# Optimization experiments

Measured on AMD Instinct MI355X. Metric: run time of the kernel, lower is better.

## Reference

```python
import jax, jax.numpy as jnp
import numpy as np

N = 8192
F_IN = 256
F_OUT = 128
SLOPE = 0.2
NEG_INF = -9000000000000000.0


def setup_inputs() -> dict:
    key = jax.random.key(0)
    k1, k2, k3, k4, k5 = jax.random.split(key, 5)
    x = jax.random.normal(k1, (N, F_IN), dtype=jnp.float32)
    adj = jax.random.randint(k2, (N, N), 0, 2).astype(jnp.float32)
    W = jax.random.normal(k3, (F_IN, F_OUT), dtype=jnp.float32) * (1.0 / np.sqrt(F_IN))
    a_src = jax.random.normal(k4, (F_OUT,), dtype=jnp.float32) * (1.0 / np.sqrt(F_OUT))
    a_dst = jax.random.normal(k5, (F_OUT,), dtype=jnp.float32) * (1.0 / np.sqrt(F_OUT))
    return {"x": x, "adj": adj, "W": W, "a_src": a_src, "a_dst": a_dst}


def reference(x, adj, W, a_src, a_dst):
    # h: (N, F_OUT)
    h = x @ W
    f_src = h @ a_src  # (N,)
    f_dst = h @ a_dst  # (N,)
    # additive attention scores: (N, N)
    e = f_src[:, None] + f_dst[None, :]
    e = jnp.where(e >= 0, e, SLOPE * e)  # leaky_relu
    e = jnp.where(adj > 0, e, NEG_INF)
    alpha = jax.nn.softmax(e, axis=1)  # (N, N)
    return alpha @ h  # (N, F_OUT)
```

## Files before the change

### kernel.cpp

```cpp
#include <hip/hip_runtime.h>
#include <hip/hip_bf16.h>

#define NN 8192
#define FIN 256
#define FO 128
#define JCHUNK 2048
#define NSTEP 32
#define L2E 1.4426950408889634f
#define C2  0.28853900817779268f

typedef __bf16 bf16x8 __attribute__((ext_vector_type(8)));
typedef __bf16 bf16x2 __attribute__((ext_vector_type(2)));
typedef float  f32x4  __attribute__((ext_vector_type(4)));

__global__ __launch_bounds__(256) void k_proj(
    const float* __restrict__ x, const float* __restrict__ W,
    const float* __restrict__ a_src, const float* __restrict__ a_dst,
    __bf16* __restrict__ Bp, float* __restrict__ f_src,
    float* __restrict__ g1, float* __restrict__ g2)
{
  __shared__ float xs[16 * FIN];
  __shared__ float fs[16], fd[16];
  const int tid = threadIdx.x;
  const int i0 = blockIdx.x * 16;

  const float4* xg = (const float4*)(x + (size_t)i0 * FIN);
  float4* xs4 = (float4*)xs;
  #pragma unroll
  for (int t = 0; t < 4; t++) xs4[tid + 256 * t] = xg[tid + 256 * t];
  if (tid < 16) { fs[tid] = 0.f; fd[tid] = 0.f; }
  __syncthreads();

  const int cq = tid & 31;
  const int rg = tid >> 5;
  const int c0 = cq * 4;
  const int r0 = rg * 2;
  float acc0[4] = {0.f,0.f,0.f,0.f};
  float acc1[4] = {0.f,0.f,0.f,0.f};
  const float* xr0 = xs + r0 * FIN;
  const float* xr1 = xs + (r0 + 1) * FIN;

  for (int k = 0; k < FIN; k += 4) {
    float4 xa = *(const float4*)(xr0 + k);
    float4 xb = *(const float4*)(xr1 + k);
    #pragma unroll
    for (int kk = 0; kk < 4; kk++) {
      float4 wv = *(const float4*)(W + (size_t)(k + kk) * FO + c0);
      float xav = ((const float*)&xa)[kk];
      float xbv = ((const float*)&xb)[kk];
      acc0[0] += xav * wv.x; acc0[1] += xav * wv.y;
      acc0[2] += xav * wv.z; acc0[3] += xav * wv.w;
      acc1[0] += xbv * wv.x; acc1[1] += xbv * wv.y;
      acc1[2] += xbv * wv.z; acc1[3] += xbv * wv.w;
    }
  }

  float4 as = *(const float4*)(a_src + c0);
  float4 ad = *(const float4*)(a_dst + c0);
  float ps0 = acc0[0]*as.x + acc0[1]*as.y + acc0[2]*as.z + acc0[3]*as.w;
  float ps1 = acc1[0]*as.x + acc1[1]*as.y + acc1[2]*as.z + acc1[3]*as.w;
  float pd0 = acc0[0]*ad.x + acc0[1]*ad.y + acc0[2]*ad.z + acc0[3]*ad.w;
  float pd1 = acc1[0]*ad.x + acc1[1]*ad.y + acc1[2]*ad.z + acc1[3]*ad.w;
  atomicAdd(&fs[r0],     ps0);
  atomicAdd(&fs[r0 + 1], ps1);
  atomicAdd(&fd[r0],     pd0);
  atomicAdd(&fd[r0 + 1], pd1);

  const int j0 = i0 + r0;
  const int kg = j0 >> 5;
  const int q  = (j0 >> 3) & 3;
  const int t0 = j0 & 7;
  #pragma unroll
  for (int c = 0; c < 4; c++) {
    const int n = c0 + c;
    bf16x2 v;
    v[0] = (__bf16)acc0[c];
    v[1] = (__bf16)acc1[c];
    size_t idx = ((size_t)(kg * 8 + (n >> 4)) * 64 + q * 16 + (n & 15)) * 8 + t0;
    *(bf16x2*)(Bp + idx) = v;
  }
  __syncthreads();
  if (tid < 16) {
    float d = fd[tid];
    f_src[i0 + tid] = fs[tid];
    g1[i0 + tid] = __builtin_amdgcn_exp2f(d * L2E);
    g2[i0 + tid] = __builtin_amdgcn_exp2f(d * C2);
  }
}

__global__ __launch_bounds__(256, 2) void k_attn(
    const float* __restrict__ adj, const __bf16* __restrict__ Bp,
    const float* __restrict__ f_src, const float* __restrict__ g1,
    const float* __restrict__ g2, float* __restrict__ out)
{
  __shared__ float accbuf[16 * FO];
  __shared__ float lred[16];
  const int tid = threadIdx.x;
  const int i0 = blockIdx.x * 16;

  ((float4*)accbuf)[tid]       = (float4){0.f, 0.f, 0.f, 0.f};
  ((float4*)accbuf)[tid + 256] = (float4){0.f, 0.f, 0.f, 0.f};
  if (tid < 16) lred[tid] = 0.f;

  const int w = tid >> 6;
  const int lane = tid & 63;
  const int m = lane & 15;
  const int q = lane >> 4;
  const int jbase = w * JCHUNK;

  const float s  = f_src[i0 + m];
  const float F1 = __builtin_amdgcn_exp2f(s * L2E);
  const float F2 = __builtin_amdgcn_exp2f(s * C2);

  f32x4 acc[8];
  #pragma unroll
  for (int t = 0; t < 8; t++) acc[t] = (f32x4){0.f, 0.f, 0.f, 0.f};
  float psum = 0.f;

  const float* adjp = adj + (size_t)(i0 + m) * NN + jbase + q * 8;
  const float* g1p = g1 + jbase + q * 8;
  const float* g2p = g2 + jbase + q * 8;
  const __bf16* bb = Bp + (size_t)(jbase >> 5) * 4096 + lane * 8;

  __syncthreads();

  float4 cur0 = *(const float4*)(adjp + 0);
  float4 cur1 = *(const float4*)(adjp + 4);
  float4 cur2 = *(const float4*)(adjp + 32);
  float4 cur3 = *(const float4*)(adjp + 36);

  #pragma unroll 2
  for (int st = 0; st < NSTEP; ++st) {
    float4 nxt0, nxt1, nxt2, nxt3;
    if (st < NSTEP - 1) {
      const float* ap = adjp + (st + 1) * 64;
      nxt0 = *(const float4*)(ap + 0);
      nxt1 = *(const float4*)(ap + 4);
      nxt2 = *(const float4*)(ap + 32);
      nxt3 = *(const float4*)(ap + 36);
    }
    #pragma unroll
    for (int g = 0; g < 2; ++g) {
      const int ko = st * 64 + g * 32;
      float4 a0 = g ? cur2 : cur0;
      float4 a1 = g ? cur3 : cur1;
      float4 u0 = *(const float4*)(g1p + ko);
      float4 u1 = *(const float4*)(g1p + ko + 4);
      float4 v0 = *(const float4*)(g2p + ko);
      float4 v1 = *(const float4*)(g2p + ko + 4);
      float p0 = (a0.x > 0.f) ? fmaxf(F1 * u0.x, F2 * v0.x) : 0.f;
      float p1 = (a0.y > 0.f) ? fmaxf(F1 * u0.y, F2 * v0.y) : 0.f;
      float p2 = (a0.z > 0.f) ? fmaxf(F1 * u0.z, F2 * v0.z) : 0.f;
      float p3 = (a0.w > 0.f) ? fmaxf(F1 * u0.w, F2 * v0.w) : 0.f;
      float p4 = (a1.x > 0.f) ? fmaxf(F1 * u1.x, F2 * v1.x) : 0.f;
      float p5 = (a1.y > 0.f) ? fmaxf(F1 * u1.y, F2 * v1.y) : 0.f;
      float p6 = (a1.z > 0.f) ? fmaxf(F1 * u1.z, F2 * v1.z) : 0.f;
      float p7 = (a1.w > 0.f) ? fmaxf(F1 * u1.w, F2 * v1.w) : 0.f;
      psum += ((p0 + p1) + (p2 + p3)) + ((p4 + p5) + (p6 + p7));

      bf16x8 af;
      af[0] = (__bf16)p0; af[1] = (__bf16)p1; af[2] = (__bf16)p2; af[3] = (__bf16)p3;
      af[4] = (__bf16)p4; af[5] = (__bf16)p5; af[6] = (__bf16)p6; af[7] = (__bf16)p7;

      const __bf16* bs = bb + (size_t)(st * 2 + g) * 4096;
      #pragma unroll
      for (int nt = 0; nt < 8; nt++) {
        bf16x8 bfrag = *(const bf16x8*)(bs + nt * 512);
        acc[nt] = __builtin_amdgcn_mfma_f32_16x16x32_bf16(af, bfrag, acc[nt], 0, 0, 0);
      }
    }
    if (st < NSTEP - 1) { cur0 = nxt0; cur1 = nxt1; cur2 = nxt2; cur3 = nxt3; }
  }

  psum += __shfl_xor(psum, 16);
  psum += __shfl_xor(psum, 32);
  if (lane < 16) atomicAdd(&lred[lane], psum);

  #pragma unroll
  for (int nt = 0; nt < 8; nt++) {
    #pragma unroll
    for (int r = 0; r < 4; r++) {
      atomicAdd(&accbuf[(q * 4 + r) * FO + nt * 16 + m], acc[nt][r]);
    }
  }
  __syncthreads();

  #pragma unroll
  for (int t = 0; t < 2; t++) {
    const int idx = tid + t * 256;
    const float inv = 1.0f / lred[idx >> 5];
    float4 v = ((const float4*)accbuf)[idx];
    float4 o;
    o.x = v.x * inv; o.y = v.y * inv; o.z = v.z * inv; o.w = v.w * inv;
    ((float4*)(out + (size_t)i0 * FO))[idx] = o;
  }
}

extern "C" void kernel_launch(void* const* d_in, const int* in_sizes, int n_in,
                              void* d_out, int out_size, void* d_ws, size_t ws_size,
                              hipStream_t stream) {
  const float* x     = (const float*)d_in[0];
  const float* adj   = (const float*)d_in[1];
  const float* W     = (const float*)d_in[2];
  const float* a_src = (const float*)d_in[3];
  const float* a_dst = (const float*)d_in[4];
  float* out = (float*)d_out;

  char* ws = (char*)d_ws;
  __bf16* Bp   = (__bf16*)ws;
  float* f_src = (float*)(ws + 2097152);
  float* g1    = (float*)(ws + 2097152 + 32768);
  float* g2    = (float*)(ws + 2097152 + 65536);

  hipLaunchKernelGGL(k_proj, dim3(512), dim3(256), 0, stream,
                     x, W, a_src, a_dst, Bp, f_src, g1, g2);
  hipLaunchKernelGGL(k_attn, dim3(512), dim3(256), 0, stream,
                     adj, Bp, f_src, g1, g2, out);
}
```

Before: 469.7 us.

## Tile attention over 64 rows with split-K across blocks and global atomic reduction

Each attention block now covers 64 rows and a quarter of the columns, so every B-fragment load from the projected features feeds four MFMAs instead of one. The g1/g2 vectors are staged in shared memory, and adj is read with nontemporal loads. Partial numerators and row sums from the four column splits are merged with global atomics into a zeroed buffer, and a new divide kernel applies the normalisation. This cuts repeated reads of the bf16 feature matrix, but adds a memset, a third kernel, float-atomic traffic, heavy register pressure from 32 accumulators, and less latency hiding for adj since the software prefetch is gone.

```diff
diff --git a/kernel.cpp b/kernel.cpp
--- a/kernel.cpp
+++ b/kernel.cpp
@@ -4,8 +4,6 @@
 #define NN 8192
 #define FIN 256
 #define FO 128
-#define JCHUNK 2048
-#define NSTEP 32
 #define L2E 1.4426950408889634f
 #define C2  0.28853900817779268f
 
@@ -91,109 +89,139 @@
 __global__ __launch_bounds__(256, 2) void k_attn(
     const float* __restrict__ adj, const __bf16* __restrict__ Bp,
     const float* __restrict__ f_src, const float* __restrict__ g1,
-    const float* __restrict__ g2, float* __restrict__ out)
+    const float* __restrict__ g2, float* __restrict__ num,
+    float* __restrict__ lsum)
 {
-  __shared__ float accbuf[16 * FO];
-  __shared__ float lred[16];
+  __shared__ float G1s[2048], G2s[2048];
+  __shared__ float accbuf[64 * FO];
+  __shared__ float lred[64];
   const int tid = threadIdx.x;
-  const int i0 = blockIdx.x * 16;
-
-  ((float4*)accbuf)[tid]       = (float4){0.f, 0.f, 0.f, 0.f};
-  ((float4*)accbuf)[tid + 256] = (float4){0.f, 0.f, 0.f, 0.f};
-  if (tid < 16) lred[tid] = 0.f;
+  const int rb = blockIdx.x >> 2;
+  const int ks = blockIdx.x & 3;
+  const int i0 = rb * 64;
+  const int cb = ks * 2048;
+
+  {
+    const float4* s1 = (const float4*)(g1 + cb);
+    const float4* s2 = (const float4*)(g2 + cb);
+    ((float4*)G1s)[tid]       = s1[tid];
+    ((float4*)G1s)[tid + 256] = s1[tid + 256];
+    ((float4*)G2s)[tid]       = s2[tid];
+    ((float4*)G2s)[tid + 256] = s2[tid + 256];
+  }
+  #pragma unroll
+  for (int t = 0; t < 8; t++)
+    ((float4*)accbuf)[tid + 256 * t] = (float4){0.f, 0.f, 0.f, 0.f};
+  if (tid < 64) lred[tid] = 0.f;
 
   const int w = tid >> 6;
   const int lane = tid & 63;
   const int m = lane & 15;
   const int q = lane >> 4;
-  const int jbase = w * JCHUNK;
-
-  const float s  = f_src[i0 + m];
-  const float F1 = __builtin_amdgcn_exp2f(s * L2E);
-  const float F2 = __builtin_amdgcn_exp2f(s * C2);
-
-  f32x4 acc[8];
-  #pragma unroll
-  for (int t = 0; t < 8; t++) acc[t] = (f32x4){0.f, 0.f, 0.f, 0.f};
-  float psum = 0.f;
-
-  const float* adjp = adj + (size_t)(i0 + m) * NN + jbase + q * 8;
-  const float* g1p = g1 + jbase + q * 8;
-  const float* g2p = g2 + jbase + q * 8;
-  const __bf16* bb = Bp + (size_t)(jbase >> 5) * 4096 + lane * 8;
-
-  __syncthreads();
-
-  float4 cur0 = *(const float4*)(adjp + 0);
-  float4 cur1 = *(const float4*)(adjp + 4);
-  float4 cur2 = *(const float4*)(adjp + 32);
-  float4 cur3 = *(const float4*)(adjp + 36);
-
-  #pragma unroll 2
-  for (int st = 0; st < NSTEP; ++st) {
-    float4 nxt0, nxt1, nxt2, nxt3;
-    if (st < NSTEP - 1) {
-      const float* ap = adjp + (st + 1) * 64;
-      nxt0 = *(const float4*)(ap + 0);
-      nxt1 = *(const float4*)(ap + 4);
-      nxt2 = *(const float4*)(ap + 32);
-      nxt3 = *(const float4*)(ap + 36);
-    }
-    #pragma unroll
-    for (int g = 0; g < 2; ++g) {
-      const int ko = st * 64 + g * 32;
-      float4 a0 = g ? cur2 : cur0;
-      float4 a1 = g ? cur3 : cur1;
-      float4 u0 = *(const float4*)(g1p + ko);
-      float4 u1 = *(const float4*)(g1p + ko + 4);
-      float4 v0 = *(const float4*)(g2p + ko);
-      float4 v1 = *(const float4*)(g2p + ko + 4);
-      float p0 = (a0.x > 0.f) ? fmaxf(F1 * u0.x, F2 * v0.x) : 0.f;
-      float p1 = (a0.y > 0.f) ? fmaxf(F1 * u0.y, F2 * v0.y) : 0.f;
-      float p2 = (a0.z > 0.f) ? fmaxf(F1 * u0.z, F2 * v0.z) : 0.f;
-      float p3 = (a0.w > 0.f) ? fmaxf(F1 * u0.w, F2 * v0.w) : 0.f;
-      float p4 = (a1.x > 0.f) ? fmaxf(F1 * u1.x, F2 * v1.x) : 0.f;
-      float p5 = (a1.y > 0.f) ? fmaxf(F1 * u1.y, F2 * v1.y) : 0.f;
-      float p6 = (a1.z > 0.f) ? fmaxf(F1 * u1.z, F2 * v1.z) : 0.f;
-      float p7 = (a1.w > 0.f) ? fmaxf(F1 * u1.w, F2 * v1.w) : 0.f;
-      psum += ((p0 + p1) + (p2 + p3)) + ((p4 + p5) + (p6 + p7));
-
-      bf16x8 af;
-      af[0] = (__bf16)p0; af[1] = (__bf16)p1; af[2] = (__bf16)p2; af[3] = (__bf16)p3;
-      af[4] = (__bf16)p4; af[5] = (__bf16)p5; af[6] = (__bf16)p6; af[7] = (__bf16)p7;
-
-      const __bf16* bs = bb + (size_t)(st * 2 + g) * 4096;
+  const int jb = cb + w * 512;
+
+  float F1[4], F2[4];
+  #pragma unroll
+  for (int mt = 0; mt < 4; mt++) {
+    float s = f_src[i0 + mt * 16 + m];
+    F1[mt] = __builtin_amdgcn_exp2f(s * L2E);
+    F2[mt] = __builtin_amdgcn_exp2f(s * C2);
+  }
+
+  f32x4 acc[4][8];
+  #pragma unroll
+  for (int mt = 0; mt < 4; mt++)
+    #pragma unroll
+    for (int nt = 0; nt < 8; nt++) acc[mt][nt] = (f32x4){0.f, 0.f, 0.f, 0.f};
+  float psum[4] = {0.f, 0.f, 0.f, 0.f};
+
+  const float* rowp[4];
+  #pragma unroll
+  for (int mt = 0; mt < 4; mt++)
+    rowp[mt] = adj + (size_t)(i0 + mt * 16 + m) * NN + jb + q * 8;
+  const __bf16* bb = Bp + (size_t)(jb >> 5) * 4096 + lane * 8;
+  const float* gl1 = G1s + w * 512 + q * 8;
+  const float* gl2 = G2s + w * 512 + q * 8;
+
+  __syncthreads();
+
+  for (int kg = 0; kg < 16; ++kg) {
+    const int ko = kg * 32;
+    f32x4 a0[4], a1[4];
+    #pragma unroll
+    for (int mt = 0; mt < 4; mt++) {
+      a0[mt] = __builtin_nontemporal_load((const f32x4*)(rowp[mt] + ko));
+      a1[mt] = __builtin_nontemporal_load((const f32x4*)(rowp[mt] + ko + 4));
+    }
+    float4 u0 = *(const float4*)(gl1 + ko);
+    float4 u1 = *(const float4*)(gl1 + ko + 4);
+    float4 v0 = *(const float4*)(gl2 + ko);
+    float4 v1 = *(const float4*)(gl2 + ko + 4);
+
+    bf16x8 af[4];
+    #pragma unroll
+    for (int mt = 0; mt < 4; mt++) {
+      const float f1 = F1[mt], f2 = F2[mt];
+      f32x4 x0 = a0[mt], x1 = a1[mt];
+      float p0 = (x0.x > 0.f) ? fmaxf(f1 * u0.x, f2 * v0.x) : 0.f;
+      float p1 = (x0.y > 0.f) ? fmaxf(f1 * u0.y, f2 * v0.y) : 0.f;
+      float p2 = (x0.z > 0.f) ? fmaxf(f1 * u0.z, f2 * v0.z) : 0.f;
+      float p3 = (x0.w > 0.f) ? fmaxf(f1 * u0.w, f2 * v0.w) : 0.f;
+      float p4 = (x1.x > 0.f) ? fmaxf(f1 * u1.x, f2 * v1.x) : 0.f;
+      float p5 = (x1.y > 0.f) ? fmaxf(f1 * u1.y, f2 * v1.y) : 0.f;
+      float p6 = (x1.z > 0.f) ? fmaxf(f1 * u1.z, f2 * v1.z) : 0.f;
+      float p7 = (x1.w > 0.f) ? fmaxf(f1 * u1.w, f2 * v1.w) : 0.f;
+      psum[mt] += ((p0 + p1) + (p2 + p3)) + ((p4 + p5) + (p6 + p7));
+      bf16x8 a;
+      a[0] = (__bf16)p0; a[1] = (__bf16)p1; a[2] = (__bf16)p2; a[3] = (__bf16)p3;
+      a[4] = (__bf16)p4; a[5] = (__bf16)p5; a[6] = (__bf16)p6; a[7] = (__bf16)p7;
+      af[mt] = a;
+    }
+
+    const __bf16* bs = bb + (size_t)kg * 4096;
+    #pragma unroll
+    for (int nt = 0; nt < 8; nt++) {
+      bf16x8 bfrag = *(const bf16x8*)(bs + nt * 512);
       #pragma unroll
-      for (int nt = 0; nt < 8; nt++) {
-        bf16x8 bfrag = *(const bf16x8*)(bs + nt * 512);
-        acc[nt] = __builtin_amdgcn_mfma_f32_16x16x32_bf16(af, bfrag, acc[nt], 0, 0, 0);
-      }
-    }
-    if (st < NSTEP - 1) { cur0 = nxt0; cur1 = nxt1; cur2 = nxt2; cur3 = nxt3; }
-  }
-
-  psum += __shfl_xor(psum, 16);
-  psum += __shfl_xor(psum, 32);
-  if (lane < 16) atomicAdd(&lred[lane], psum);
-
-  #pragma unroll
-  for (int nt = 0; nt < 8; nt++) {
-    #pragma unroll
-    for (int r = 0; r < 4; r++) {
-      atomicAdd(&accbuf[(q * 4 + r) * FO + nt * 16 + m], acc[nt][r]);
-    }
-  }
-  __syncthreads();
-
-  #pragma unroll
-  for (int t = 0; t < 2; t++) {
-    const int idx = tid + t * 256;
-    const float inv = 1.0f / lred[idx >> 5];
-    float4 v = ((const float4*)accbuf)[idx];
-    float4 o;
-    o.x = v.x * inv; o.y = v.y * inv; o.z = v.z * inv; o.w = v.w * inv;
-    ((float4*)(out + (size_t)i0 * FO))[idx] = o;
-  }
+      for (int mt = 0; mt < 4; mt++)
+        acc[mt][nt] = __builtin_amdgcn_mfma_f32_16x16x32_bf16(af[mt], bfrag, acc[mt][nt], 0, 0, 0);
+    }
+  }
+
+  #pragma unroll
+  for (int mt = 0; mt < 4; mt++) {
+    float p = psum[mt];
+    p += __shfl_xor(p, 16);
+    p += __shfl_xor(p, 32);
+    if (lane < 16) atomicAdd(&lred[mt * 16 + lane], p);
+  }
+
+  #pragma unroll
+  for (int mt = 0; mt < 4; mt++)
+    #pragma unroll
+    for (int nt = 0; nt < 8; nt++)
+      #pragma unroll
+      for (int r = 0; r < 4; r++)
+        atomicAdd(&accbuf[(mt * 16 + q * 4 + r) * FO + nt * 16 + m], acc[mt][nt][r]);
+  __syncthreads();
+
+  float* nb = num + (size_t)i0 * FO;
+  #pragma unroll
+  for (int t = 0; t < 32; t++)
+    atomicAdd(&nb[tid + 256 * t], accbuf[tid + 256 * t]);
+  if (tid < 64) atomicAdd(&lsum[i0 + tid], lred[tid]);
+}
+
+__global__ __launch_bounds__(256) void k_div(
+    const float* __restrict__ num, const float* __restrict__ lsum,
+    float* __restrict__ out)
+{
+  int idx = blockIdx.x * 256 + threadIdx.x;
+  float4 v = ((const float4*)num)[idx];
+  float inv = 1.0f / lsum[idx >> 5];
+  float4 o;
+  o.x = v.x * inv; o.y = v.y * inv; o.z = v.z * inv; o.w = v.w * inv;
+  ((float4*)out)[idx] = o;
 }
 
 extern "C" void kernel_launch(void* const* d_in, const int* in_sizes, int n_in,
@@ -211,9 +239,14 @@
   float* f_src = (float*)(ws + 2097152);
   float* g1    = (float*)(ws + 2097152 + 32768);
   float* g2    = (float*)(ws + 2097152 + 65536);
-
+  float* num   = (float*)(ws + 2097152 + 98304);
+  float* lsum  = (float*)(ws + 2097152 + 98304 + 4194304);
+
+  hipMemsetAsync(num, 0, 4194304 + 32768, stream);
   hipLaunchKernelGGL(k_proj, dim3(512), dim3(256), 0, stream,
                      x, W, a_src, a_dst, Bp, f_src, g1, g2);
   hipLaunchKernelGGL(k_attn, dim3(512), dim3(256), 0, stream,
-                     adj, Bp, f_src, g1, g2, out);
-}
+                     adj, Bp, f_src, g1, g2, num, lsum);
+  hipLaunchKernelGGL(k_div, dim3(1024), dim3(256), 0, stream,
+                     num, lsum, out);
+}
```

Result: slower. 555.3 us (+18.2%).
